# Optimization experiments

Hardware: AMD Instinct MI355X
Metric: run time of the kernel (lower is better)

Reference implementation:

```python
import jax, jax.numpy as jnp
import numpy as np

D_MODEL = 1024
H = 16
D_K = D_MODEL // H


def setup_inputs() -> dict:
    key = jax.random.key(0)
    ks = jax.random.split(key, 11)
    B, S = 4, 2048
    scale = 1.0 / np.sqrt(D_MODEL)
    inp = {
        "q": jax.random.normal(ks[0], (B, S, D_MODEL), jnp.float32),
        "k": jax.random.normal(ks[1], (B, S, D_MODEL), jnp.float32),
        "v": jax.random.normal(ks[2], (B, S, D_MODEL), jnp.float32),
        # Linear weights stored as (in, out) so y = x @ W + b
        "W_q": jax.random.normal(ks[3], (D_MODEL, D_MODEL), jnp.float32) * scale,
        "b_q": jnp.zeros((D_MODEL,), jnp.float32),
        "W_k": jax.random.normal(ks[4], (D_MODEL, D_MODEL), jnp.float32) * scale,
        "b_k": jnp.zeros((D_MODEL,), jnp.float32),
        "W_v": jax.random.normal(ks[5], (D_MODEL, D_MODEL), jnp.float32) * scale,
        "b_v": jnp.zeros((D_MODEL,), jnp.float32),
        "W_o": jax.random.normal(ks[6], (D_MODEL, D_MODEL), jnp.float32) * scale,
        "b_o": jnp.zeros((D_MODEL,), jnp.float32),
    }
    return inp


def _split_heads(x, B):
    # (B, S, d_model) -> (B, h, S, d_k)
    return x.reshape(B, -1, H, D_K).transpose(0, 2, 1, 3)


def reference(q, k, v, W_q, b_q, W_k, b_k, W_v, b_v, W_o, b_o):
    B = q.shape[0]
    qh = _split_heads(q @ W_q + b_q, B)  # (B,h,S,dk)
    kh = _split_heads(k @ W_k + b_k, B)
    vh = _split_heads(v @ W_v + b_v, B)
    scores = jnp.einsum("bhsd,bhtd->bhst", qh, kh) / jnp.sqrt(jnp.float32(D_K))
    attn = jax.nn.softmax(scores, axis=-1)  # dropout p=0 -> identity
    out = jnp.einsum("bhst,bhtd->bhsd", attn, vh)  # (B,h,S,dk)
    out = out.transpose(0, 2, 1, 3).reshape(B, -1, H * D_K)  # merge heads
    return out @ W_o + b_o
```

## Files before the change

### kernel.cpp

```cpp
#include <hip/hip_runtime.h>

#define D_MODEL 1024
#define SEQ 2048
#define BATCH 4
#define NHEADS 16
#define HDK 64
#define MTOT (BATCH * SEQ)
#define NT (SEQ / 64)

typedef __attribute__((ext_vector_type(8))) _Float16 f16x8;
typedef __attribute__((ext_vector_type(2))) __fp16 pk16x2;
typedef __attribute__((ext_vector_type(4))) float f32x4;

__device__ inline unsigned short f2h_bits(float f) {
  _Float16 h = (_Float16)f;
  union { _Float16 h; unsigned short u; } c;
  c.h = h;
  return c.u;
}

__device__ inline unsigned pk2(float a, float b) {
  union { pk16x2 h; unsigned u; } c;
  c.h = __builtin_amdgcn_cvt_pkrtz(a, b);
  return c.u;
}

__global__ __launch_bounds__(256) void wtrans_kernel(
    const float* __restrict__ W0, const float* __restrict__ W1,
    const float* __restrict__ W2, const float* __restrict__ W3,
    unsigned short* __restrict__ WT) {
  __shared__ float tile[64][65];
  const float* W = blockIdx.z == 0 ? W0 : blockIdx.z == 1 ? W1
                  : blockIdx.z == 2 ? W2 : W3;
  unsigned short* out = WT + (size_t)blockIdx.z * D_MODEL * D_MODEL;
  const int k0 = blockIdx.x * 64, n0 = blockIdx.y * 64;
  const int t = threadIdx.x;
#pragma unroll
  for (int i = 0; i < 16; ++i) {
    int e = t + i * 256;
    int r = e >> 6, c = e & 63;
    tile[r][c] = W[(size_t)(k0 + r) * D_MODEL + n0 + c];
  }
  __syncthreads();
#pragma unroll
  for (int i = 0; i < 16; ++i) {
    int e = t + i * 256;
    int r = e >> 6, c = e & 63;
    out[(size_t)(n0 + r) * D_MODEL + k0 + c] = f2h_bits(tile[c][r]);
  }
}

template <bool A_F32, int OUT_MODE>
__global__ __launch_bounds__(256) void gemm_kernel(
    const void* __restrict__ Aptr, const unsigned short* __restrict__ Bt,
    const float* __restrict__ bias, void* __restrict__ Cptr) {
  __shared__ unsigned short As[128 * 64];
  __shared__ unsigned short Bs[128 * 64];
  const int t = threadIdx.x;
  const int lane = t & 63, w = t >> 6;
  const int lo16 = lane & 15, g = lane >> 4;
  const int wr = w >> 1, wc = w & 1;
  const int m0 = blockIdx.x * 128, n0 = blockIdx.y * 128;

  f32x4 acc[4][4] = {};

  for (int kt = 0; kt < D_MODEL / 64; ++kt) {
    if constexpr (A_F32) {
      const float* Af = (const float*)Aptr;
#pragma unroll
      for (int i = 0; i < 8; ++i) {
        int e4 = t + i * 256;
        int row = e4 >> 4, c4 = e4 & 15;
        float4 vv = *reinterpret_cast<const float4*>(
            Af + (size_t)(m0 + row) * D_MODEL + kt * 64 + c4 * 4);
        int kq = c4 * 4;
        int slot = (kq >> 3) ^ (row & 7);
        ushort4 p;
        p.x = f2h_bits(vv.x); p.y = f2h_bits(vv.y);
        p.z = f2h_bits(vv.z); p.w = f2h_bits(vv.w);
        *reinterpret_cast<ushort4*>(&As[row * 64 + slot * 8 + (kq & 7)]) = p;
      }
    } else {
      const unsigned short* Ah = (const unsigned short*)Aptr;
#pragma unroll
      for (int i = 0; i < 4; ++i) {
        int e8 = t + i * 256;
        int row = e8 >> 3, c8 = e8 & 7;
        int4 vv = *reinterpret_cast<const int4*>(
            Ah + (size_t)(m0 + row) * D_MODEL + kt * 64 + c8 * 8);
        int slot = c8 ^ (row & 7);
        *reinterpret_cast<int4*>(&As[row * 64 + slot * 8]) = vv;
      }
    }
#pragma unroll
    for (int i = 0; i < 4; ++i) {
      int e8 = t + i * 256;
      int row = e8 >> 3, c8 = e8 & 7;
      int4 vv = *reinterpret_cast<const int4*>(
          Bt + (size_t)(n0 + row) * D_MODEL + kt * 64 + c8 * 8);
      int slot = c8 ^ (row & 7);
      *reinterpret_cast<int4*>(&Bs[row * 64 + slot * 8]) = vv;
    }
    __syncthreads();

#pragma unroll
    for (int kk = 0; kk < 2; ++kk) {
      f16x8 af[4], bfr[4];
#pragma unroll
      for (int m = 0; m < 4; ++m) {
        int row = wr * 64 + m * 16 + lo16;
        int slot = (kk * 4 + g) ^ (row & 7);
        af[m] = *reinterpret_cast<const f16x8*>(&As[row * 64 + slot * 8]);
      }
#pragma unroll
      for (int n = 0; n < 4; ++n) {
        int row = wc * 64 + n * 16 + lo16;
        int slot = (kk * 4 + g) ^ (row & 7);
        bfr[n] = *reinterpret_cast<const f16x8*>(&Bs[row * 64 + slot * 8]);
      }
#pragma unroll
      for (int m = 0; m < 4; ++m)
#pragma unroll
        for (int n = 0; n < 4; ++n)
          acc[m][n] = __builtin_amdgcn_mfma_f32_16x16x32_f16(af[m], bfr[n],
                                                             acc[m][n], 0, 0, 0);
    }
    __syncthreads();
  }

#pragma unroll
  for (int m = 0; m < 4; ++m) {
#pragma unroll
    for (int n = 0; n < 4; ++n) {
      int col = n0 + wc * 64 + n * 16 + lo16;
      float bv = bias[col];
      if constexpr (OUT_MODE == 2) {
        int hh = col >> 6, dk = col & 63;
        int r = m0 + wr * 64 + m * 16 + g * 4;
        int bb = r >> 11, ss = r & 2047;
        ushort4 pkv;
        pkv.x = f2h_bits(acc[m][n][0] + bv);
        pkv.y = f2h_bits(acc[m][n][1] + bv);
        pkv.z = f2h_bits(acc[m][n][2] + bv);
        pkv.w = f2h_bits(acc[m][n][3] + bv);
        *reinterpret_cast<ushort4*>(
            (unsigned short*)Cptr +
            (((size_t)bb * NHEADS + hh) * HDK + dk) * SEQ + ss) = pkv;
      } else {
#pragma unroll
        for (int j = 0; j < 4; ++j) {
          int row = m0 + wr * 64 + m * 16 + g * 4 + j;
          float val = acc[m][n][j] + bv;
          if constexpr (OUT_MODE == 1) {
            ((float*)Cptr)[(size_t)row * D_MODEL + col] = val;
          } else {
            ((unsigned short*)Cptr)[(size_t)row * D_MODEL + col] = f2h_bits(val);
          }
        }
      }
    }
  }
}

__global__ __launch_bounds__(256, 3) void attn_kernel(
    const unsigned short* __restrict__ QP, const unsigned short* __restrict__ KP,
    const unsigned short* __restrict__ VPT, unsigned short* __restrict__ CTX) {
  __shared__ unsigned short Kb[2][64 * 64];
  __shared__ unsigned short Vb[2][64 * 64];
  const int t = threadIdx.x;
  const int lane = t & 63, w = t >> 6;
  const int lo16 = lane & 15, g = lane >> 4;
  const int b = blockIdx.z, h = blockIdx.y;
  const int q0 = blockIdx.x * 128;
  const size_t rowbase = (size_t)b * SEQ;
  const int bh = b * NHEADS + h;

  f16x8 qf[2][2];
#pragma unroll
  for (int nQ = 0; nQ < 2; ++nQ)
#pragma unroll
    for (int kk = 0; kk < 2; ++kk) {
      qf[nQ][kk] = *reinterpret_cast<const f16x8*>(
          QP + (rowbase + q0 + w * 32 + nQ * 16 + lo16) * D_MODEL + h * 64 +
          kk * 32 + g * 8);
      qf[nQ][kk] *= (_Float16)0.18033688f;
    }

  f32x4 o_acc[2][4] = {};
  float lsum[2] = {0.f, 0.f};

  const int r0 = t >> 3, c8i = t & 7;
  const unsigned short* kg0 =
      KP + (rowbase + r0) * D_MODEL + h * 64 + c8i * 8;
  const unsigned short* kg1 = kg0 + (size_t)32 * D_MODEL;
  const unsigned short* vg0 =
      VPT + ((size_t)bh * HDK + r0) * SEQ + c8i * 8;
  const unsigned short* vg1 = vg0 + (size_t)32 * SEQ;
  const int so0 = r0 * 64 + ((c8i ^ (r0 & 7)) * 8);
  const int so1 = (r0 + 32) * 64 + ((c8i ^ (r0 & 7)) * 8);

  {
    int4 k0v = *reinterpret_cast<const int4*>(kg0);
    int4 k1v = *reinterpret_cast<const int4*>(kg1);
    int4 v0v = *reinterpret_cast<const int4*>(vg0);
    int4 v1v = *reinterpret_cast<const int4*>(vg1);
    *reinterpret_cast<int4*>(&Kb[0][so0]) = k0v;
    *reinterpret_cast<int4*>(&Kb[0][so1]) = k1v;
    *reinterpret_cast<int4*>(&Vb[0][so0]) = v0v;
    *reinterpret_cast<int4*>(&Vb[0][so1]) = v1v;
  }
  kg0 += (size_t)64 * D_MODEL; kg1 += (size_t)64 * D_MODEL;
  vg0 += 64; vg1 += 64;
  __syncthreads();

  const bool evn = ((g & 1) == 0);
  const bool lowp = (g < 2);
  const bool isg0 = (g == 0), isg3 = (g == 3);
  int cur = 0;

  for (int kt = 0; kt < NT; ++kt) {
    int4 kreg[2], vreg[2];
    if (kt + 1 < NT) {
      kreg[0] = *reinterpret_cast<const int4*>(kg0);
      kreg[1] = *reinterpret_cast<const int4*>(kg1);
      vreg[0] = *reinterpret_cast<const int4*>(vg0);
      vreg[1] = *reinterpret_cast<const int4*>(vg1);
      kg0 += (size_t)64 * D_MODEL; kg1 += (size_t)64 * D_MODEL;
      vg0 += 64; vg1 += 64;
    }

    const unsigned short* Ksh = Kb[cur];
    const unsigned short* Vsh = Vb[cur];

    f32x4 s[4][2] = {};
#pragma unroll
    for (int kk = 0; kk < 2; ++kk) {
      f16x8 kf[4];
#pragma unroll
      for (int mK = 0; mK < 4; ++mK)
        kf[mK] = *reinterpret_cast<const f16x8*>(
            &Ksh[(mK * 16 + lo16) * 64 + (((kk * 4 + g) ^ (lo16 & 7)) * 8)]);
#pragma unroll
      for (int mK = 0; mK < 4; ++mK)
#pragma unroll
        for (int nQ = 0; nQ < 2; ++nQ)
          s[mK][nQ] = __builtin_amdgcn_mfma_f32_16x16x32_f16(
              kf[mK], qf[nQ][kk], s[mK][nQ], 0, 0, 0);
    }

#pragma unroll
    for (int nQ = 0; nQ < 2; ++nQ) {
#pragma unroll
      for (int mK = 0; mK < 4; ++mK)
#pragma unroll
        for (int j = 0; j < 4; ++j)
          s[mK][nQ][j] = __builtin_amdgcn_exp2f(s[mK][nQ][j]);
      f32x4 sm = (s[0][nQ] + s[1][nQ]) + (s[2][nQ] + s[3][nQ]);
      lsum[nQ] += (sm[0] + sm[1]) + (sm[2] + sm[3]);
    }

#pragma unroll
    for (int kk = 0; kk < 2; ++kk) {
      f16x8 pf[2];
#pragma unroll
      for (int mA = 0; mA < 2; ++mA) {
        unsigned L0 = pk2(s[2 * kk][mA][0], s[2 * kk][mA][1]);
        unsigned L1 = pk2(s[2 * kk][mA][2], s[2 * kk][mA][3]);
        unsigned H0 = pk2(s[2 * kk + 1][mA][0], s[2 * kk + 1][mA][1]);
        unsigned H1 = pk2(s[2 * kk + 1][mA][2], s[2 * kk + 1][mA][3]);
        unsigned L0x = __shfl_xor(L0, 16), L1x = __shfl_xor(L1, 16);
        unsigned H0x = __shfl_xor(H0, 16), H1x = __shfl_xor(H1, 16);
        unsigned EL0 = evn ? L0 : L0x, EL1 = evn ? L1 : L1x;
        unsigned OL0 = evn ? L0x : L0, OL1 = evn ? L1x : L1;
        unsigned EH0 = evn ? H0 : H0x, EH1 = evn ? H1 : H1x;
        unsigned OH0 = evn ? H0x : H0, OH1 = evn ? H1x : H1;
        unsigned R0 = __shfl_xor(lowp ? EH0 : EL0, 32);
        unsigned R1 = __shfl_xor(lowp ? EH1 : EL1, 32);
        unsigned R2 = __shfl_xor(lowp ? OH0 : OL0, 32);
        unsigned R3 = __shfl_xor(lowp ? OH1 : OL1, 32);
        unsigned W0 = isg0 ? EL0 : (isg3 ? EH0 : R0);
        unsigned W1 = isg0 ? EL1 : (isg3 ? EH1 : R1);
        unsigned W2 = isg0 ? OL0 : (isg3 ? OH0 : R2);
        unsigned W3 = isg0 ? OL1 : (isg3 ? OH1 : R3);
        union { uint4 u; f16x8 h; } cv;
        cv.u = make_uint4(W0, W1, W2, W3);
        pf[mA] = cv.h;
      }
      f16x8 vf[4];
#pragma unroll
      for (int n4 = 0; n4 < 4; ++n4)
        vf[n4] = *reinterpret_cast<const f16x8*>(
            &Vsh[(n4 * 16 + lo16) * 64 + (((kk * 4 + g) ^ (lo16 & 7)) * 8)]);
#pragma unroll
      for (int mA = 0; mA < 2; ++mA)
#pragma unroll
        for (int n4 = 0; n4 < 4; ++n4)
          o_acc[mA][n4] = __builtin_amdgcn_mfma_f32_16x16x32_f16(
              pf[mA], vf[n4], o_acc[mA][n4], 0, 0, 0);
    }

    if (kt + 1 < NT) {
      unsigned short* Kn = Kb[cur ^ 1];
      unsigned short* Vn = Vb[cur ^ 1];
      *reinterpret_cast<int4*>(&Kn[so0]) = kreg[0];
      *reinterpret_cast<int4*>(&Kn[so1]) = kreg[1];
      *reinterpret_cast<int4*>(&Vn[so0]) = vreg[0];
      *reinterpret_cast<int4*>(&Vn[so1]) = vreg[1];
    }
    __syncthreads();
    cur ^= 1;
  }

#pragma unroll
  for (int nQ = 0; nQ < 2; ++nQ) {
    lsum[nQ] += __shfl_xor(lsum[nQ], 16);
    lsum[nQ] += __shfl_xor(lsum[nQ], 32);
  }
  float li[2][4];
#pragma unroll
  for (int mA = 0; mA < 2; ++mA)
#pragma unroll
    for (int j = 0; j < 4; ++j)
      li[mA][j] = 1.0f / __shfl(lsum[mA], g * 4 + j);
#pragma unroll
  for (int mA = 0; mA < 2; ++mA)
#pragma unroll
    for (int n4 = 0; n4 < 4; ++n4)
#pragma unroll
      for (int j = 0; j < 4; ++j) {
        size_t row = rowbase + q0 + w * 32 + mA * 16 + g * 4 + j;
        CTX[row * D_MODEL + h * 64 + n4 * 16 + lo16] =
            f2h_bits(o_acc[mA][n4][j] * li[mA][j]);
      }
}

extern "C" void kernel_launch(void* const* d_in, const int* in_sizes, int n_in,
                              void* d_out, int out_size, void* d_ws,
                              size_t ws_size, hipStream_t stream) {
  (void)in_sizes; (void)n_in; (void)out_size; (void)ws_size;
  const float* q  = (const float*)d_in[0];
  const float* k  = (const float*)d_in[1];
  const float* v  = (const float*)d_in[2];
  const float* Wq = (const float*)d_in[3];
  const float* bq = (const float*)d_in[4];
  const float* Wk = (const float*)d_in[5];
  const float* bk = (const float*)d_in[6];
  const float* Wv = (const float*)d_in[7];
  const float* bv = (const float*)d_in[8];
  const float* Wo = (const float*)d_in[9];
  const float* bo = (const float*)d_in[10];

  unsigned short* WT  = (unsigned short*)d_ws;
  unsigned short* QP  = WT + (size_t)4 * D_MODEL * D_MODEL;
  unsigned short* KP  = QP + (size_t)MTOT * D_MODEL;
  unsigned short* VPT = KP + (size_t)MTOT * D_MODEL;
  unsigned short* CTX = VPT + (size_t)MTOT * D_MODEL;

  wtrans_kernel<<<dim3(16, 16, 4), 256, 0, stream>>>(Wq, Wk, Wv, Wo, WT);

  dim3 gg(MTOT / 128, D_MODEL / 128);
  gemm_kernel<true, 0><<<gg, 256, 0, stream>>>(
      q, WT + (size_t)0 * D_MODEL * D_MODEL, bq, QP);
  gemm_kernel<true, 0><<<gg, 256, 0, stream>>>(
      k, WT + (size_t)1 * D_MODEL * D_MODEL, bk, KP);
  gemm_kernel<true, 2><<<gg, 256, 0, stream>>>(
      v, WT + (size_t)2 * D_MODEL * D_MODEL, bv, VPT);

  attn_kernel<<<dim3(SEQ / 128, NHEADS, BATCH), 256, 0, stream>>>(QP, KP, VPT, CTX);

  gemm_kernel<false, 1><<<gg, 256, 0, stream>>>(
      CTX, WT + (size_t)3 * D_MODEL * D_MODEL, bo, d_out);
}
```

Baseline: 235.5 us.

## Use direct global-to-LDS loads with pre-swizzled layouts and triple-buffered attention pipeline

Producers (weight transpose, K projection, V projection, attention output) now write fp16 data in the XOR-swizzled order that consumers expect. Consumers can then use global_load_lds 16-byte copies straight into shared memory, with no register staging. The attention kernel switches to three K/V buffers and software-pipelines QK^T of the next tile against softmax/PV of the current one. Grids are flattened and remapped to change block order for locality, and the f32 A path uses packed fp16 conversion. The cost is more LDS per attention block, which may lower occupancy, plus extra register pressure from two score arrays.

Result: slower. 275.9 us (+17.1%).

```diff
diff --git a/kernel.cpp b/kernel.cpp
--- a/kernel.cpp
+++ b/kernel.cpp
@@ -23,6 +23,12 @@
   union { pk16x2 h; unsigned u; } c;
   c.h = __builtin_amdgcn_cvt_pkrtz(a, b);
   return c.u;
+}
+
+typedef __attribute__((address_space(3))) unsigned int lds_u32_t;
+typedef __attribute__((address_space(1))) const unsigned int glb_u32_t;
+__device__ __forceinline__ void gll16(const void* g, void* l) {
+  __builtin_amdgcn_global_load_lds((glb_u32_t*)g, (lds_u32_t*)l, 16, 0, 0);
 }
 
 __global__ __launch_bounds__(256) void wtrans_kernel(
@@ -46,11 +52,13 @@
   for (int i = 0; i < 16; ++i) {
     int e = t + i * 256;
     int r = e >> 6, c = e & 63;
-    out[(size_t)(n0 + r) * D_MODEL + k0 + c] = f2h_bits(tile[c][r]);
-  }
-}
-
-template <bool A_F32, int OUT_MODE>
+    int slot = (c >> 3) ^ (r & 7);
+    out[(size_t)(n0 + r) * D_MODEL + k0 + slot * 8 + (c & 7)] =
+        f2h_bits(tile[c][r]);
+  }
+}
+
+template <int A_MODE, int OUT_MODE>
 __global__ __launch_bounds__(256) void gemm_kernel(
     const void* __restrict__ Aptr, const unsigned short* __restrict__ Bt,
     const float* __restrict__ bias, void* __restrict__ Cptr) {
@@ -60,47 +68,44 @@
   const int lane = t & 63, w = t >> 6;
   const int lo16 = lane & 15, g = lane >> 4;
   const int wr = w >> 1, wc = w & 1;
-  const int m0 = blockIdx.x * 128, n0 = blockIdx.y * 128;
+  const int bx = blockIdx.x >> 3, by = blockIdx.x & 7;
+  const int m0 = bx * 128, n0 = by * 128;
 
   f32x4 acc[4][4] = {};
 
+  const unsigned short* bgb =
+      Bt + (size_t)(n0 + (t >> 3)) * D_MODEL + (t & 7) * 8;
+  const float* agf = nullptr;
+  const unsigned short* agh = nullptr;
+  if constexpr (A_MODE == 0)
+    agf = (const float*)Aptr + (size_t)(m0 + (t >> 4)) * D_MODEL + (t & 15) * 4;
+  else
+    agh = (const unsigned short*)Aptr + (size_t)(m0 + (t >> 3)) * D_MODEL +
+          (t & 7) * 8;
+
   for (int kt = 0; kt < D_MODEL / 64; ++kt) {
-    if constexpr (A_F32) {
-      const float* Af = (const float*)Aptr;
+    if constexpr (A_MODE == 0) {
 #pragma unroll
       for (int i = 0; i < 8; ++i) {
-        int e4 = t + i * 256;
-        int row = e4 >> 4, c4 = e4 & 15;
-        float4 vv = *reinterpret_cast<const float4*>(
-            Af + (size_t)(m0 + row) * D_MODEL + kt * 64 + c4 * 4);
-        int kq = c4 * 4;
+        int row = (t >> 4) + i * 16, kq = (t & 15) * 4;
+        float4 vv = *reinterpret_cast<const float4*>(agf + (size_t)i * 16 * D_MODEL);
         int slot = (kq >> 3) ^ (row & 7);
-        ushort4 p;
-        p.x = f2h_bits(vv.x); p.y = f2h_bits(vv.y);
-        p.z = f2h_bits(vv.z); p.w = f2h_bits(vv.w);
-        *reinterpret_cast<ushort4*>(&As[row * 64 + slot * 8 + (kq & 7)]) = p;
-      }
+        uint2 pp;
+        pp.x = pk2(vv.x, vv.y);
+        pp.y = pk2(vv.z, vv.w);
+        *reinterpret_cast<uint2*>(&As[row * 64 + slot * 8 + (kq & 7)]) = pp;
+      }
+      agf += 64;
     } else {
-      const unsigned short* Ah = (const unsigned short*)Aptr;
-#pragma unroll
-      for (int i = 0; i < 4; ++i) {
-        int e8 = t + i * 256;
-        int row = e8 >> 3, c8 = e8 & 7;
-        int4 vv = *reinterpret_cast<const int4*>(
-            Ah + (size_t)(m0 + row) * D_MODEL + kt * 64 + c8 * 8);
-        int slot = c8 ^ (row & 7);
-        *reinterpret_cast<int4*>(&As[row * 64 + slot * 8]) = vv;
-      }
-    }
-#pragma unroll
-    for (int i = 0; i < 4; ++i) {
-      int e8 = t + i * 256;
-      int row = e8 >> 3, c8 = e8 & 7;
-      int4 vv = *reinterpret_cast<const int4*>(
-          Bt + (size_t)(n0 + row) * D_MODEL + kt * 64 + c8 * 8);
-      int slot = c8 ^ (row & 7);
-      *reinterpret_cast<int4*>(&Bs[row * 64 + slot * 8]) = vv;
-    }
+#pragma unroll
+      for (int i = 0; i < 4; ++i)
+        gll16(agh + (size_t)i * 32 * D_MODEL, &As[(size_t)(i * 256 + t) * 8]);
+      agh += 64;
+    }
+#pragma unroll
+    for (int i = 0; i < 4; ++i)
+      gll16(bgb + (size_t)i * 32 * D_MODEL, &Bs[(size_t)(i * 256 + t) * 8]);
+    bgb += 64;
     __syncthreads();
 
 #pragma unroll
@@ -138,6 +143,7 @@
         int hh = col >> 6, dk = col & 63;
         int r = m0 + wr * 64 + m * 16 + g * 4;
         int bb = r >> 11, ss = r & 2047;
+        int ssw = (ss & ~63) + ((((ss >> 3) & 7) ^ (dk & 7)) << 3) + (ss & 7);
         ushort4 pkv;
         pkv.x = f2h_bits(acc[m][n][0] + bv);
         pkv.y = f2h_bits(acc[m][n][1] + bv);
@@ -145,7 +151,16 @@
         pkv.w = f2h_bits(acc[m][n][3] + bv);
         *reinterpret_cast<ushort4*>(
             (unsigned short*)Cptr +
-            (((size_t)bb * NHEADS + hh) * HDK + dk) * SEQ + ss) = pkv;
+            (((size_t)bb * NHEADS + hh) * HDK + dk) * SEQ + ssw) = pkv;
+      } else if constexpr (OUT_MODE == 3) {
+        int colbase = col & ~63, c8 = (col >> 3) & 7, c1 = col & 7;
+#pragma unroll
+        for (int j = 0; j < 4; ++j) {
+          int row = m0 + wr * 64 + m * 16 + g * 4 + j;
+          int colp = colbase + ((c8 ^ ((g * 4 + j) & 7)) << 3) + c1;
+          ((unsigned short*)Cptr)[(size_t)row * D_MODEL + colp] =
+              f2h_bits(acc[m][n][j] + bv);
+        }
       } else {
 #pragma unroll
         for (int j = 0; j < 4; ++j) {
@@ -165,15 +180,15 @@
 __global__ __launch_bounds__(256, 3) void attn_kernel(
     const unsigned short* __restrict__ QP, const unsigned short* __restrict__ KP,
     const unsigned short* __restrict__ VPT, unsigned short* __restrict__ CTX) {
-  __shared__ unsigned short Kb[2][64 * 64];
-  __shared__ unsigned short Vb[2][64 * 64];
+  __shared__ unsigned short Kb[3][64 * 64];
+  __shared__ unsigned short Vb[3][64 * 64];
   const int t = threadIdx.x;
   const int lane = t & 63, w = t >> 6;
   const int lo16 = lane & 15, g = lane >> 4;
-  const int b = blockIdx.z, h = blockIdx.y;
-  const int q0 = blockIdx.x * 128;
+  const int bh = blockIdx.x & 63, qt = blockIdx.x >> 6;
+  const int b = bh >> 4, h = bh & 15;
+  const int q0 = qt * 128;
   const size_t rowbase = (size_t)b * SEQ;
-  const int bh = b * NHEADS + h;
 
   f16x8 qf[2][2];
 #pragma unroll
@@ -189,50 +204,36 @@
   f32x4 o_acc[2][4] = {};
   float lsum[2] = {0.f, 0.f};
 
-  const int r0 = t >> 3, c8i = t & 7;
-  const unsigned short* kg0 =
-      KP + (rowbase + r0) * D_MODEL + h * 64 + c8i * 8;
-  const unsigned short* kg1 = kg0 + (size_t)32 * D_MODEL;
-  const unsigned short* vg0 =
-      VPT + ((size_t)bh * HDK + r0) * SEQ + c8i * 8;
-  const unsigned short* vg1 = vg0 + (size_t)32 * SEQ;
-  const int so0 = r0 * 64 + ((c8i ^ (r0 & 7)) * 8);
-  const int so1 = (r0 + 32) * 64 + ((c8i ^ (r0 & 7)) * 8);
-
-  {
-    int4 k0v = *reinterpret_cast<const int4*>(kg0);
-    int4 k1v = *reinterpret_cast<const int4*>(kg1);
-    int4 v0v = *reinterpret_cast<const int4*>(vg0);
-    int4 v1v = *reinterpret_cast<const int4*>(vg1);
-    *reinterpret_cast<int4*>(&Kb[0][so0]) = k0v;
-    *reinterpret_cast<int4*>(&Kb[0][so1]) = k1v;
-    *reinterpret_cast<int4*>(&Vb[0][so0]) = v0v;
-    *reinterpret_cast<int4*>(&Vb[0][so1]) = v1v;
-  }
-  kg0 += (size_t)64 * D_MODEL; kg1 += (size_t)64 * D_MODEL;
-  vg0 += 64; vg1 += 64;
+  const unsigned short* kgb =
+      KP + (rowbase + (t >> 3)) * D_MODEL + h * 64 + (t & 7) * 8;
+  const unsigned short* vgb =
+      VPT + ((size_t)bh * HDK + (t >> 3)) * SEQ + (t & 7) * 8;
+
+#pragma unroll
+  for (int i = 0; i < 2; ++i) {
+    gll16(kgb + (size_t)i * 32 * D_MODEL, &Kb[0][(size_t)(i * 256 + t) * 8]);
+    gll16(vgb + (size_t)i * 32 * SEQ, &Vb[0][(size_t)(i * 256 + t) * 8]);
+  }
+  kgb += (size_t)64 * D_MODEL; vgb += 64;
+#pragma unroll
+  for (int i = 0; i < 2; ++i) {
+    gll16(kgb + (size_t)i * 32 * D_MODEL, &Kb[1][(size_t)(i * 256 + t) * 8]);
+    gll16(vgb + (size_t)i * 32 * SEQ, &Vb[1][(size_t)(i * 256 + t) * 8]);
+  }
+  kgb += (size_t)64 * D_MODEL; vgb += 64;
   __syncthreads();
 
   const bool evn = ((g & 1) == 0);
   const bool lowp = (g < 2);
   const bool isg0 = (g == 0), isg3 = (g == 3);
-  int cur = 0;
-
-  for (int kt = 0; kt < NT; ++kt) {
-    int4 kreg[2], vreg[2];
-    if (kt + 1 < NT) {
-      kreg[0] = *reinterpret_cast<const int4*>(kg0);
-      kreg[1] = *reinterpret_cast<const int4*>(kg1);
-      vreg[0] = *reinterpret_cast<const int4*>(vg0);
-      vreg[1] = *reinterpret_cast<const int4*>(vg1);
-      kg0 += (size_t)64 * D_MODEL; kg1 += (size_t)64 * D_MODEL;
-      vg0 += 64; vg1 += 64;
-    }
-
-    const unsigned short* Ksh = Kb[cur];
-    const unsigned short* Vsh = Vb[cur];
-
-    f32x4 s[4][2] = {};
+
+  f32x4 sA[4][2], sB[4][2];
+
+  auto qkt = [&](const unsigned short* Ksh, f32x4 (&sd)[4][2]) {
+#pragma unroll
+    for (int mK = 0; mK < 4; ++mK)
+#pragma unroll
+      for (int nQ = 0; nQ < 2; ++nQ) sd[mK][nQ] = f32x4{0.f, 0.f, 0.f, 0.f};
 #pragma unroll
     for (int kk = 0; kk < 2; ++kk) {
       f16x8 kf[4];
@@ -244,9 +245,23 @@
       for (int mK = 0; mK < 4; ++mK)
 #pragma unroll
         for (int nQ = 0; nQ < 2; ++nQ)
-          s[mK][nQ] = __builtin_amdgcn_mfma_f32_16x16x32_f16(
-              kf[mK], qf[nQ][kk], s[mK][nQ], 0, 0, 0);
-    }
+          sd[mK][nQ] = __builtin_amdgcn_mfma_f32_16x16x32_f16(
+              kf[mK], qf[nQ][kk], sd[mK][nQ], 0, 0, 0);
+    }
+  };
+
+  auto body = [&](int tl, f32x4 (&scur)[4][2], f32x4 (&snxt)[4][2], int iv,
+                  int ik, int iw) {
+    if (tl + 2 < NT) {
+#pragma unroll
+      for (int i = 0; i < 2; ++i) {
+        gll16(kgb + (size_t)i * 32 * D_MODEL,
+              &Kb[iw][(size_t)(i * 256 + t) * 8]);
+        gll16(vgb + (size_t)i * 32 * SEQ, &Vb[iw][(size_t)(i * 256 + t) * 8]);
+      }
+      kgb += (size_t)64 * D_MODEL; vgb += 64;
+    }
+    if (tl + 1 < NT) qkt(&Kb[ik][0], snxt);
 
 #pragma unroll
     for (int nQ = 0; nQ < 2; ++nQ) {
@@ -254,20 +269,21 @@
       for (int mK = 0; mK < 4; ++mK)
 #pragma unroll
         for (int j = 0; j < 4; ++j)
-          s[mK][nQ][j] = __builtin_amdgcn_exp2f(s[mK][nQ][j]);
-      f32x4 sm = (s[0][nQ] + s[1][nQ]) + (s[2][nQ] + s[3][nQ]);
+          scur[mK][nQ][j] = __builtin_amdgcn_exp2f(scur[mK][nQ][j]);
+      f32x4 sm = (scur[0][nQ] + scur[1][nQ]) + (scur[2][nQ] + scur[3][nQ]);
       lsum[nQ] += (sm[0] + sm[1]) + (sm[2] + sm[3]);
     }
 
+    const unsigned short* Vsh = &Vb[iv][0];
 #pragma unroll
     for (int kk = 0; kk < 2; ++kk) {
       f16x8 pf[2];
 #pragma unroll
       for (int mA = 0; mA < 2; ++mA) {
-        unsigned L0 = pk2(s[2 * kk][mA][0], s[2 * kk][mA][1]);
-        unsigned L1 = pk2(s[2 * kk][mA][2], s[2 * kk][mA][3]);
-        unsigned H0 = pk2(s[2 * kk + 1][mA][0], s[2 * kk + 1][mA][1]);
-        unsigned H1 = pk2(s[2 * kk + 1][mA][2], s[2 * kk + 1][mA][3]);
+        unsigned L0 = pk2(scur[2 * kk][mA][0], scur[2 * kk][mA][1]);
+        unsigned L1 = pk2(scur[2 * kk][mA][2], scur[2 * kk][mA][3]);
+        unsigned H0 = pk2(scur[2 * kk + 1][mA][0], scur[2 * kk + 1][mA][1]);
+        unsigned H1 = pk2(scur[2 * kk + 1][mA][2], scur[2 * kk + 1][mA][3]);
         unsigned L0x = __shfl_xor(L0, 16), L1x = __shfl_xor(L1, 16);
         unsigned H0x = __shfl_xor(H0, 16), H1x = __shfl_xor(H1, 16);
         unsigned EL0 = evn ? L0 : L0x, EL1 = evn ? L1 : L1x;
@@ -298,17 +314,17 @@
           o_acc[mA][n4] = __builtin_amdgcn_mfma_f32_16x16x32_f16(
               pf[mA], vf[n4], o_acc[mA][n4], 0, 0, 0);
     }
-
-    if (kt + 1 < NT) {
-      unsigned short* Kn = Kb[cur ^ 1];
-      unsigned short* Vn = Vb[cur ^ 1];
-      *reinterpret_cast<int4*>(&Kn[so0]) = kreg[0];
-      *reinterpret_cast<int4*>(&Kn[so1]) = kreg[1];
-      *reinterpret_cast<int4*>(&Vn[so0]) = vreg[0];
-      *reinterpret_cast<int4*>(&Vn[so1]) = vreg[1];
-    }
     __syncthreads();
-    cur ^= 1;
+  };
+
+  qkt(&Kb[0][0], sA);
+
+  int iv = 0, ik = 1, iw = 2;
+  for (int tp = 0; tp < NT; tp += 2) {
+    body(tp, sA, sB, iv, ik, iw);
+    { int x = iv; iv = ik; ik = iw; iw = x; }
+    body(tp + 1, sB, sA, iv, ik, iw);
+    { int x = iv; iv = ik; ik = iw; iw = x; }
   }
 
 #pragma unroll
@@ -325,13 +341,16 @@
 #pragma unroll
   for (int mA = 0; mA < 2; ++mA)
 #pragma unroll
-    for (int n4 = 0; n4 < 4; ++n4)
+    for (int n4 = 0; n4 < 4; ++n4) {
+      int c8 = ((n4 * 16 + lo16) >> 3) & 7, c1 = lo16 & 7;
 #pragma unroll
       for (int j = 0; j < 4; ++j) {
         size_t row = rowbase + q0 + w * 32 + mA * 16 + g * 4 + j;
-        CTX[row * D_MODEL + h * 64 + n4 * 16 + lo16] =
+        int tok7 = (g * 4 + j) & 7;
+        CTX[row * D_MODEL + h * 64 + ((c8 ^ tok7) << 3) + c1] =
             f2h_bits(o_acc[mA][n4][j] * li[mA][j]);
       }
+    }
 }
 
 extern "C" void kernel_launch(void* const* d_in, const int* in_sizes, int n_in,
@@ -358,16 +377,15 @@
 
   wtrans_kernel<<<dim3(16, 16, 4), 256, 0, stream>>>(Wq, Wk, Wv, Wo, WT);
 
-  dim3 gg(MTOT / 128, D_MODEL / 128);
-  gemm_kernel<true, 0><<<gg, 256, 0, stream>>>(
+  gemm_kernel<0, 0><<<512, 256, 0, stream>>>(
       q, WT + (size_t)0 * D_MODEL * D_MODEL, bq, QP);
-  gemm_kernel<true, 0><<<gg, 256, 0, stream>>>(
+  gemm_kernel<0, 3><<<512, 256, 0, stream>>>(
       k, WT + (size_t)1 * D_MODEL * D_MODEL, bk, KP);
-  gemm_kernel<true, 2><<<gg, 256, 0, stream>>>(
+  gemm_kernel<0, 2><<<512, 256, 0, stream>>>(
       v, WT + (size_t)2 * D_MODEL * D_MODEL, bv, VPT);
 
-  attn_kernel<<<dim3(SEQ / 128, NHEADS, BATCH), 256, 0, stream>>>(QP, KP, VPT, CTX);
-
-  gemm_kernel<false, 1><<<gg, 256, 0, stream>>>(
+  attn_kernel<<<1024, 256, 0, stream>>>(QP, KP, VPT, CTX);
+
+  gemm_kernel<1, 1><<<512, 256, 0, stream>>>(
       CTX, WT + (size_t)3 * D_MODEL * D_MODEL, bo, d_out);
 }
```

## Double-buffer GEMM global loads with 512-thread blocks and reorder attention grid

Applied to the files above, without the earlier changes.

The GEMM kernel now runs 8 waves per block, each owning a 64x32 output tile, and prefetches the next K tile into registers while MFMAs run on the current shared-memory tile. This is meant to hide global-load latency and to spread the f32-to-f16 conversion, now done with packed conversions, across more threads. The attention launch becomes a 1D grid with batch-head index fastest, so blocks sharing K/V run close together for better cache reuse. The cost is an extra barrier per K step and more registers held for the prefetch.

Measured after the change: 385.5 us. +63.7%, slower.

```diff
diff --git a/kernel.cpp b/kernel.cpp
--- a/kernel.cpp
+++ b/kernel.cpp
@@ -51,7 +51,7 @@
 }
 
 template <bool A_F32, int OUT_MODE>
-__global__ __launch_bounds__(256) void gemm_kernel(
+__global__ __launch_bounds__(512, 4) void gemm_kernel(
     const void* __restrict__ Aptr, const unsigned short* __restrict__ Bt,
     const float* __restrict__ bias, void* __restrict__ Cptr) {
   __shared__ unsigned short As[128 * 64];
@@ -59,53 +59,89 @@
   const int t = threadIdx.x;
   const int lane = t & 63, w = t >> 6;
   const int lo16 = lane & 15, g = lane >> 4;
-  const int wr = w >> 1, wc = w & 1;
+  const int wr = w >> 2, wc = w & 3;
   const int m0 = blockIdx.x * 128, n0 = blockIdx.y * 128;
 
-  f32x4 acc[4][4] = {};
+  f32x4 acc[4][2] = {};
+
+  const float* agf = nullptr;
+  const unsigned short* agh = nullptr;
+  int arow, akq, aso[4];
+  if constexpr (A_F32) {
+    arow = t >> 4; akq = (t & 15) * 4;
+    agf = (const float*)Aptr + (size_t)(m0 + arow) * D_MODEL + akq;
+#pragma unroll
+    for (int i = 0; i < 4; ++i) {
+      int row = arow + i * 32;
+      aso[i] = row * 64 + (((akq >> 3) ^ (row & 7)) * 8) + (akq & 7);
+    }
+  } else {
+    arow = t >> 3; akq = (t & 7) * 8;
+    agh = (const unsigned short*)Aptr + (size_t)(m0 + arow) * D_MODEL + akq;
+#pragma unroll
+    for (int i = 0; i < 2; ++i) {
+      int row = arow + i * 64;
+      aso[i] = row * 64 + ((((akq >> 3)) ^ (row & 7)) * 8);
+    }
+  }
+  const int brow = t >> 3, bc8 = t & 7;
+  const unsigned short* bgb =
+      Bt + (size_t)(n0 + brow) * D_MODEL + bc8 * 8;
+  int bso[2];
+#pragma unroll
+  for (int i = 0; i < 2; ++i) {
+    int row = brow + i * 64;
+    bso[i] = row * 64 + ((bc8 ^ (row & 7)) * 8);
+  }
+
+  if constexpr (A_F32) {
+#pragma unroll
+    for (int i = 0; i < 4; ++i) {
+      float4 vv = *reinterpret_cast<const float4*>(agf + (size_t)i * 32 * D_MODEL);
+      uint2 pp; pp.x = pk2(vv.x, vv.y); pp.y = pk2(vv.z, vv.w);
+      *reinterpret_cast<uint2*>(&As[aso[i]]) = pp;
+    }
+    agf += 64;
+  } else {
+#pragma unroll
+    for (int i = 0; i < 2; ++i) {
+      int4 vv = *reinterpret_cast<const int4*>(agh + (size_t)i * 64 * D_MODEL);
+      *reinterpret_cast<int4*>(&As[aso[i]]) = vv;
+    }
+    agh += 64;
+  }
+#pragma unroll
+  for (int i = 0; i < 2; ++i) {
+    int4 vv = *reinterpret_cast<const int4*>(bgb + (size_t)i * 64 * D_MODEL);
+    *reinterpret_cast<int4*>(&Bs[bso[i]]) = vv;
+  }
+  bgb += 64;
+  __syncthreads();
 
   for (int kt = 0; kt < D_MODEL / 64; ++kt) {
-    if constexpr (A_F32) {
-      const float* Af = (const float*)Aptr;
-#pragma unroll
-      for (int i = 0; i < 8; ++i) {
-        int e4 = t + i * 256;
-        int row = e4 >> 4, c4 = e4 & 15;
-        float4 vv = *reinterpret_cast<const float4*>(
-            Af + (size_t)(m0 + row) * D_MODEL + kt * 64 + c4 * 4);
-        int kq = c4 * 4;
-        int slot = (kq >> 3) ^ (row & 7);
-        ushort4 p;
-        p.x = f2h_bits(vv.x); p.y = f2h_bits(vv.y);
-        p.z = f2h_bits(vv.z); p.w = f2h_bits(vv.w);
-        *reinterpret_cast<ushort4*>(&As[row * 64 + slot * 8 + (kq & 7)]) = p;
-      }
-    } else {
-      const unsigned short* Ah = (const unsigned short*)Aptr;
-#pragma unroll
-      for (int i = 0; i < 4; ++i) {
-        int e8 = t + i * 256;
-        int row = e8 >> 3, c8 = e8 & 7;
-        int4 vv = *reinterpret_cast<const int4*>(
-            Ah + (size_t)(m0 + row) * D_MODEL + kt * 64 + c8 * 8);
-        int slot = c8 ^ (row & 7);
-        *reinterpret_cast<int4*>(&As[row * 64 + slot * 8]) = vv;
-      }
-    }
-#pragma unroll
-    for (int i = 0; i < 4; ++i) {
-      int e8 = t + i * 256;
-      int row = e8 >> 3, c8 = e8 & 7;
-      int4 vv = *reinterpret_cast<const int4*>(
-          Bt + (size_t)(n0 + row) * D_MODEL + kt * 64 + c8 * 8);
-      int slot = c8 ^ (row & 7);
-      *reinterpret_cast<int4*>(&Bs[row * 64 + slot * 8]) = vv;
-    }
-    __syncthreads();
+    float4 apf[4]; int4 ahf[2]; int4 bpf[2];
+    const bool have = (kt + 1 < D_MODEL / 64);
+    if (have) {
+      if constexpr (A_F32) {
+#pragma unroll
+        for (int i = 0; i < 4; ++i)
+          apf[i] = *reinterpret_cast<const float4*>(agf + (size_t)i * 32 * D_MODEL);
+        agf += 64;
+      } else {
+#pragma unroll
+        for (int i = 0; i < 2; ++i)
+          ahf[i] = *reinterpret_cast<const int4*>(agh + (size_t)i * 64 * D_MODEL);
+        agh += 64;
+      }
+#pragma unroll
+      for (int i = 0; i < 2; ++i)
+        bpf[i] = *reinterpret_cast<const int4*>(bgb + (size_t)i * 64 * D_MODEL);
+      bgb += 64;
+    }
 
 #pragma unroll
     for (int kk = 0; kk < 2; ++kk) {
-      f16x8 af[4], bfr[4];
+      f16x8 af[4], bfr[2];
 #pragma unroll
       for (int m = 0; m < 4; ++m) {
         int row = wr * 64 + m * 16 + lo16;
@@ -113,26 +149,44 @@
         af[m] = *reinterpret_cast<const f16x8*>(&As[row * 64 + slot * 8]);
       }
 #pragma unroll
-      for (int n = 0; n < 4; ++n) {
-        int row = wc * 64 + n * 16 + lo16;
+      for (int n = 0; n < 2; ++n) {
+        int row = wc * 32 + n * 16 + lo16;
         int slot = (kk * 4 + g) ^ (row & 7);
         bfr[n] = *reinterpret_cast<const f16x8*>(&Bs[row * 64 + slot * 8]);
       }
 #pragma unroll
       for (int m = 0; m < 4; ++m)
 #pragma unroll
-        for (int n = 0; n < 4; ++n)
+        for (int n = 0; n < 2; ++n)
           acc[m][n] = __builtin_amdgcn_mfma_f32_16x16x32_f16(af[m], bfr[n],
                                                              acc[m][n], 0, 0, 0);
     }
     __syncthreads();
+
+    if (have) {
+      if constexpr (A_F32) {
+#pragma unroll
+        for (int i = 0; i < 4; ++i) {
+          uint2 pp; pp.x = pk2(apf[i].x, apf[i].y); pp.y = pk2(apf[i].z, apf[i].w);
+          *reinterpret_cast<uint2*>(&As[aso[i]]) = pp;
+        }
+      } else {
+#pragma unroll
+        for (int i = 0; i < 2; ++i)
+          *reinterpret_cast<int4*>(&As[aso[i]]) = ahf[i];
+      }
+#pragma unroll
+      for (int i = 0; i < 2; ++i)
+        *reinterpret_cast<int4*>(&Bs[bso[i]]) = bpf[i];
+    }
+    __syncthreads();
   }
 
 #pragma unroll
   for (int m = 0; m < 4; ++m) {
 #pragma unroll
-    for (int n = 0; n < 4; ++n) {
-      int col = n0 + wc * 64 + n * 16 + lo16;
+    for (int n = 0; n < 2; ++n) {
+      int col = n0 + wc * 32 + n * 16 + lo16;
       float bv = bias[col];
       if constexpr (OUT_MODE == 2) {
         int hh = col >> 6, dk = col & 63;
@@ -170,10 +224,10 @@
   const int t = threadIdx.x;
   const int lane = t & 63, w = t >> 6;
   const int lo16 = lane & 15, g = lane >> 4;
-  const int b = blockIdx.z, h = blockIdx.y;
-  const int q0 = blockIdx.x * 128;
+  const int bh = blockIdx.x & 63, qt = blockIdx.x >> 6;
+  const int b = bh >> 4, h = bh & 15;
+  const int q0 = qt * 128;
   const size_t rowbase = (size_t)b * SEQ;
-  const int bh = b * NHEADS + h;
 
   f16x8 qf[2][2];
 #pragma unroll
@@ -359,15 +413,15 @@
   wtrans_kernel<<<dim3(16, 16, 4), 256, 0, stream>>>(Wq, Wk, Wv, Wo, WT);
 
   dim3 gg(MTOT / 128, D_MODEL / 128);
-  gemm_kernel<true, 0><<<gg, 256, 0, stream>>>(
+  gemm_kernel<true, 0><<<gg, 512, 0, stream>>>(
       q, WT + (size_t)0 * D_MODEL * D_MODEL, bq, QP);
-  gemm_kernel<true, 0><<<gg, 256, 0, stream>>>(
+  gemm_kernel<true, 0><<<gg, 512, 0, stream>>>(
       k, WT + (size_t)1 * D_MODEL * D_MODEL, bk, KP);
-  gemm_kernel<true, 2><<<gg, 256, 0, stream>>>(
+  gemm_kernel<true, 2><<<gg, 512, 0, stream>>>(
       v, WT + (size_t)2 * D_MODEL * D_MODEL, bv, VPT);
 
-  attn_kernel<<<dim3(SEQ / 128, NHEADS, BATCH), 256, 0, stream>>>(QP, KP, VPT, CTX);
-
-  gemm_kernel<false, 1><<<gg, 256, 0, stream>>>(
+  attn_kernel<<<1024, 256, 0, stream>>>(QP, KP, VPT, CTX);
+
+  gemm_kernel<false, 1><<<gg, 512, 0, stream>>>(
       CTX, WT + (size_t)3 * D_MODEL * D_MODEL, bo, d_out);
 }
```
